# Kernel optimization log

Measured on AMD Instinct MI355X. Metric: run time of the kernel, lower is better.

## Reference

```python
import jax, jax.numpy as jnp
import numpy as np


def setup_inputs() -> dict:
    key = jax.random.key(0)
    k1, k2 = jax.random.split(key)
    b, c, h, w = 2, 128, 96, 128
    feature0 = jax.random.normal(k1, (b, c, h, w), dtype=jnp.float32)
    feature1 = jax.random.normal(k2, (b, c, h, w), dtype=jnp.float32)
    return {"feature0": feature0, "feature1": feature1, "local_radius": 4}


def reference(feature0, feature1, local_radius):
    # Faithful to the torch module: sample coords are base pixel coords + integer
    # window offsets, so align_corners=True bilinear grid_sample with zeros padding
    # reduces exactly to an integer gather with out-of-bounds masking.
    b, c, h, w = feature0.shape
    r = int(local_radius)
    # base pixel coords (x, y), matching coords_grid channel order
    ys, xs = jnp.meshgrid(jnp.arange(h, dtype=jnp.float32),
                          jnp.arange(w, dtype=jnp.float32), indexing='ij')  # [h,w]
    # window offsets; row-major over (dy, dx) like generate_window_grid reshape(-1,2)
    dy, dx = jnp.meshgrid(jnp.arange(-r, r + 1), jnp.arange(-r, r + 1), indexing='ij')
    dy = dy.reshape(-1).astype(jnp.float32)  # [K]
    dx = dx.reshape(-1).astype(jnp.float32)
    K = dx.shape[0]

    sample_x = xs[:, :, None] + dx  # [h,w,K]
    sample_y = ys[:, :, None] + dy
    valid = ((sample_x >= 0) & (sample_x <= w - 1) &
             (sample_y >= 0) & (sample_y <= h - 1))  # [h,w,K]

    cxi = jnp.clip(sample_x, 0, w - 1).astype(jnp.int32)
    cyi = jnp.clip(sample_y, 0, h - 1).astype(jnp.int32)
    # gather: [b,c,h,w,K]; zeros padding outside bounds
    window_feature = feature1[:, :, cyi, cxi] * valid.astype(feature1.dtype)

    # correlation: per-pixel [1,c] x [c,K]
    corr = jnp.einsum('bchw,bchwk->bhwk', feature0, window_feature) / (c ** 0.5)
    prob = jax.nn.softmax(corr, axis=-1)  # [b,h,w,K]

    # weighted coord sum -> correspondence, then flow = correspondence - coords
    corr_x = jnp.sum(prob * sample_x, axis=-1)  # [b,h,w]
    corr_y = jnp.sum(prob * sample_y, axis=-1)
    flow = jnp.stack([corr_x - xs, corr_y - ys], axis=1)  # [b,2,h,w]

    match_prob = prob.reshape(b, h * w, K)
    return flow, match_prob
```

## Files before the change

kernel.cpp:

```cpp
#include <hip/hip_runtime.h>
#include <math.h>

#define W_ 128
#define H_ 96
#define C_ 128
#define HW_ (H_ * W_)
#define K_ 81
#define FLOW_ELEMS (2 * 2 * H_ * W_)
#define TCOLS 32
#define TSTR 66

typedef __fp16 f16x8 __attribute__((ext_vector_type(8)));
typedef float  f32x4 __attribute__((ext_vector_type(4)));

__device__ __forceinline__ unsigned pack_pair(float a, float b) {
    return __builtin_bit_cast(unsigned, __builtin_amdgcn_cvt_pkrtz(a, b));
}

__global__ __launch_bounds__(192) void fused_kernel(const float* __restrict__ f0,
                                                    const float* __restrict__ f1,
                                                    float* __restrict__ out) {
    __shared__ unsigned tile[TCOLS * TSTR];
    __shared__ float corr_lds[3][16][85];
    __shared__ float pmax[4][49], psum[4][49], pfxb[4][49], pfyb[4][49];
    __shared__ float ibuf[48];

    const int t = threadIdx.x;
    const int ry = t >> 6, l = t & 63;
    const int L = (blockIdx.x & 7) * 64 + (blockIdx.x >> 3);
    const int b = L >> 8;
    const int rem = L & 255;
    const int ys = rem >> 3, xq = rem & 7;
    const int y0 = ys * 3;
    const int px0 = xq * 16;

    int g_off[2], lds_w[2];
    bool g_ok[2];
#pragma unroll
    for (int i = 0; i < 2; ++i) {
        const int s = i * 192 + t;
        const int cp = s / 6;
        const int q = s - cp * 6;
        const int x0 = px0 + 4 * q - 4;
        g_ok[i] = (x0 >= 0) && (x0 <= 124);
        g_off[i] = 2 * cp * HW_ + (g_ok[i] ? x0 : 0);
        lds_w[i] = (4 * q) * TSTR + cp;
    }
    const float* f1base = f1 + (size_t)b * C_ * HW_;

    const float scale = 0.08838834764831845f;
    f16x8 a[4];
    {
        const float* f0p = f0 + (size_t)b * C_ * HW_ + (size_t)(y0 + ry) * W_
                              + px0 + (l & 15);
#pragma unroll
        for (int kk = 0; kk < 4; ++kk) {
            f16x8 av;
#pragma unroll
            for (int j = 0; j < 8; ++j)
                av[j] = (__fp16)(f0p[(size_t)(kk * 32 + (l >> 4) * 8 + j) * HW_] * scale);
            a[kk] = av;
        }
    }

    auto LOADP = [&](int p, float4 (&va)[2], float4 (&vb)[2], bool& ok) {
        const int r = y0 - 4 + p;
        ok = (r >= 0) && (r < H_);
        const float* f1b = f1base + (size_t)(ok ? r : 0) * W_;
#pragma unroll
        for (int i = 0; i < 2; ++i) {
            float4 x = {0.f, 0.f, 0.f, 0.f}, y = {0.f, 0.f, 0.f, 0.f};
            if (ok && g_ok[i]) {
                x = *(const float4*)(f1b + g_off[i]);
                y = *(const float4*)(f1b + g_off[i] + HW_);
            }
            va[i] = x; vb[i] = y;
        }
    };
    auto WRITEP = [&](const float4 (&va)[2], const float4 (&vb)[2]) {
#pragma unroll
        for (int i = 0; i < 2; ++i) {
            tile[lds_w[i]]            = pack_pair(va[i].x, vb[i].x);
            tile[lds_w[i] + TSTR]     = pack_pair(va[i].y, vb[i].y);
            tile[lds_w[i] + 2 * TSTR] = pack_pair(va[i].z, vb[i].z);
            tile[lds_w[i] + 3 * TSTR] = pack_pair(va[i].w, vb[i].w);
        }
    };
    auto COMPUTE = [&](int dyi) {
        f32x4 accA = {0.f, 0.f, 0.f, 0.f}, accB = {0.f, 0.f, 0.f, 0.f};
#pragma unroll
        for (int kk = 0; kk < 4; ++kk) {
            const int off = kk * 16 + (l >> 4) * 4;
            {
                const int col = l & 15;
                const uint2 lo = *(const uint2*)&tile[col * TSTR + off];
                const uint2 hi = *(const uint2*)&tile[col * TSTR + off + 2];
                const uint4 u = {lo.x, lo.y, hi.x, hi.y};
                accA = __builtin_amdgcn_mfma_f32_16x16x32_f16(
                    a[kk], __builtin_bit_cast(f16x8, u), accA, 0, 0, 0);
            }
            {
                const int col = 16 + (l & 15);
                const uint2 lo = *(const uint2*)&tile[col * TSTR + off];
                const uint2 hi = *(const uint2*)&tile[col * TSTR + off + 2];
                const uint4 u = {lo.x, lo.y, hi.x, hi.y};
                accB = __builtin_amdgcn_mfma_f32_16x16x32_f16(
                    a[kk], __builtin_bit_cast(f16x8, u), accB, 0, 0, 0);
            }
        }
#pragma unroll
        for (int h = 0; h < 2; ++h) {
            const f32x4 acc = h ? accB : accA;
#pragma unroll
            for (int rg = 0; rg < 4; ++rg) {
                const int i2 = (l >> 4) * 4 + rg;
                const int j2 = h * 16 + (l & 15);
                const int dxw = j2 - i2;
                if (dxw >= 0 && dxw <= 8)
                    corr_lds[ry][i2][dyi * 9 + dxw] = acc[rg];
            }
        }
    };

    float4 vaA[2], vbA[2], vaB[2], vbB[2], vaC[2], vbC[2];
    bool okA, okB, okC;

    LOADP(0, vaA, vbA, okA);
    LOADP(1, vaB, vbB, okB);
    for (int i = t; i < 3 * 16 * 85; i += 192) (&corr_lds[0][0][0])[i] = 0.f;
    __syncthreads();

#define PHASE(p, VA, VB, OK, LP, NVA, NVB, NOK)                              \
    do {                                                                     \
        if (OK) WRITEP(VA, VB);                                              \
        __syncthreads();                                                     \
        if (LP <= 10) LOADP(LP, NVA, NVB, NOK);                              \
        const int dyi = (p) - ry;                                            \
        if (OK && dyi >= 0 && dyi <= 8) COMPUTE(dyi);                        \
        __syncthreads();                                                     \
    } while (0)

    PHASE(0, vaA, vbA, okA, 2, vaC, vbC, okC);
    PHASE(1, vaB, vbB, okB, 3, vaA, vbA, okA);
    PHASE(2, vaC, vbC, okC, 4, vaB, vbB, okB);
    PHASE(3, vaA, vbA, okA, 5, vaC, vbC, okC);
    PHASE(4, vaB, vbB, okB, 6, vaA, vbA, okA);
    PHASE(5, vaC, vbC, okC, 7, vaB, vbB, okB);
    PHASE(6, vaA, vbA, okA, 8, vaC, vbC, okC);
    PHASE(7, vaB, vbB, okB, 9, vaA, vbA, okA);
    PHASE(8, vaC, vbC, okC, 10, vaB, vbB, okB);
    PHASE(9, vaA, vbA, okA, 11, vaC, vbC, okC);
    PHASE(10, vaB, vbB, okB, 11, vaC, vbC, okC);
#undef PHASE

    {
        const int pxi = t % 48;
        const int part = t / 48;
        const int sry = pxi >> 4, spx = pxi & 15;
        float pm = -1e30f;
        for (int k = part; k < K_; k += 4)
            pm = fmaxf(pm, corr_lds[sry][spx][k]);
        pmax[part][pxi] = pm;
        __syncthreads();
        const float m = fmaxf(fmaxf(pmax[0][pxi], pmax[1][pxi]),
                              fmaxf(pmax[2][pxi], pmax[3][pxi]));
        float ps = 0.f, pfx = 0.f, pfy = 0.f;
        for (int k = part; k < K_; k += 4) {
            const float e = __expf(corr_lds[sry][spx][k] - m);
            corr_lds[sry][spx][k] = e;
            ps += e;
            pfx += e * (float)(k % 9 - 4);
            pfy += e * (float)(k / 9 - 4);
        }
        psum[part][pxi] = ps; pfxb[part][pxi] = pfx; pfyb[part][pxi] = pfy;
        __syncthreads();
        if (t < 48) {
            const float s = psum[0][t] + psum[1][t] + psum[2][t] + psum[3][t];
            const float inv = 1.f / s;
            ibuf[t] = inv;
            const float fx = pfxb[0][t] + pfxb[1][t] + pfxb[2][t] + pfxb[3][t];
            const float fy = pfyb[0][t] + pfyb[1][t] + pfyb[2][t] + pfyb[3][t];
            const int yy = y0 + (t >> 4);
            const int x = px0 + (t & 15);
            out[((size_t)(b * 2 + 0) * H_ + yy) * W_ + x] = fx * inv;
            out[((size_t)(b * 2 + 1) * H_ + yy) * W_ + x] = fy * inv;
        }
    }
    __syncthreads();

    float* outp = out + FLOW_ELEMS;
    for (int f = t; f < 48 * K_; f += 192) {
        const int pxi = f / K_;
        const int k = f - pxi * K_;
        const int yy = y0 + (pxi >> 4);
        const int x = px0 + (pxi & 15);
        outp[((size_t)b * HW_ + (size_t)yy * W_ + x) * K_ + k] =
            corr_lds[pxi >> 4][pxi & 15][k] * ibuf[pxi];
    }
}

extern "C" void kernel_launch(void* const* d_in, const int* in_sizes, int n_in,
                              void* d_out, int out_size, void* d_ws, size_t ws_size,
                              hipStream_t stream) {
    (void)in_sizes; (void)n_in; (void)out_size; (void)d_ws; (void)ws_size;
    const float* f0 = (const float*)d_in[0];
    const float* f1 = (const float*)d_in[1];
    float* out = (float*)d_out;

    fused_kernel<<<512, 192, 0, stream>>>(f0, f1, out);
}
```

Measured before the change: 22.65 us.

## Double-buffer LDS tile and deepen global prefetch to five rows

Makes the shared tile two buffers that alternate between phases, which removes the second barrier in each phase. It also raises the register prefetch depth from two rows to five, so global loads of f1 run further ahead of the MFMA compute. WRITEP now always writes, relying on LOADP zero-filling out-of-range rows, and compute is guarded by the row range instead. The cost is more registers (ten float4 pairs) and extra LDS, which may lower occupancy.

```diff
diff --git a/kernel.cpp b/kernel.cpp
--- a/kernel.cpp
+++ b/kernel.cpp
@@ -20,7 +20,7 @@
 __global__ __launch_bounds__(192) void fused_kernel(const float* __restrict__ f0,
                                                     const float* __restrict__ f1,
                                                     float* __restrict__ out) {
-    __shared__ unsigned tile[TCOLS * TSTR];
+    __shared__ unsigned tile[2][TCOLS * TSTR];
     __shared__ float corr_lds[3][16][85];
     __shared__ float pmax[4][49], psum[4][49], pfxb[4][49], pfyb[4][49];
     __shared__ float ibuf[48];
@@ -63,9 +63,9 @@
         }
     }
 
-    auto LOADP = [&](int p, float4 (&va)[2], float4 (&vb)[2], bool& ok) {
+    auto LOADP = [&](int p, float4 (&va)[2], float4 (&vb)[2]) {
         const int r = y0 - 4 + p;
-        ok = (r >= 0) && (r < H_);
+        const bool ok = (r >= 0) && (r < H_);
         const float* f1b = f1base + (size_t)(ok ? r : 0) * W_;
 #pragma unroll
         for (int i = 0; i < 2; ++i) {
@@ -77,32 +77,32 @@
             va[i] = x; vb[i] = y;
         }
     };
-    auto WRITEP = [&](const float4 (&va)[2], const float4 (&vb)[2]) {
+    auto WRITEP = [&](unsigned* tl, const float4 (&va)[2], const float4 (&vb)[2]) {
 #pragma unroll
         for (int i = 0; i < 2; ++i) {
-            tile[lds_w[i]]            = pack_pair(va[i].x, vb[i].x);
-            tile[lds_w[i] + TSTR]     = pack_pair(va[i].y, vb[i].y);
-            tile[lds_w[i] + 2 * TSTR] = pack_pair(va[i].z, vb[i].z);
-            tile[lds_w[i] + 3 * TSTR] = pack_pair(va[i].w, vb[i].w);
+            tl[lds_w[i]]            = pack_pair(va[i].x, vb[i].x);
+            tl[lds_w[i] + TSTR]     = pack_pair(va[i].y, vb[i].y);
+            tl[lds_w[i] + 2 * TSTR] = pack_pair(va[i].z, vb[i].z);
+            tl[lds_w[i] + 3 * TSTR] = pack_pair(va[i].w, vb[i].w);
         }
     };
-    auto COMPUTE = [&](int dyi) {
+    auto COMPUTE = [&](const unsigned* tl, int dyi) {
         f32x4 accA = {0.f, 0.f, 0.f, 0.f}, accB = {0.f, 0.f, 0.f, 0.f};
 #pragma unroll
         for (int kk = 0; kk < 4; ++kk) {
             const int off = kk * 16 + (l >> 4) * 4;
             {
                 const int col = l & 15;
-                const uint2 lo = *(const uint2*)&tile[col * TSTR + off];
-                const uint2 hi = *(const uint2*)&tile[col * TSTR + off + 2];
+                const uint2 lo = *(const uint2*)&tl[col * TSTR + off];
+                const uint2 hi = *(const uint2*)&tl[col * TSTR + off + 2];
                 const uint4 u = {lo.x, lo.y, hi.x, hi.y};
                 accA = __builtin_amdgcn_mfma_f32_16x16x32_f16(
                     a[kk], __builtin_bit_cast(f16x8, u), accA, 0, 0, 0);
             }
             {
                 const int col = 16 + (l & 15);
-                const uint2 lo = *(const uint2*)&tile[col * TSTR + off];
-                const uint2 hi = *(const uint2*)&tile[col * TSTR + off + 2];
+                const uint2 lo = *(const uint2*)&tl[col * TSTR + off];
+                const uint2 hi = *(const uint2*)&tl[col * TSTR + off + 2];
                 const uint4 u = {lo.x, lo.y, hi.x, hi.y};
                 accB = __builtin_amdgcn_mfma_f32_16x16x32_f16(
                     a[kk], __builtin_bit_cast(f16x8, u), accB, 0, 0, 0);
@@ -122,36 +122,41 @@
         }
     };
 
-    float4 vaA[2], vbA[2], vaB[2], vbB[2], vaC[2], vbC[2];
-    bool okA, okB, okC;
-
-    LOADP(0, vaA, vbA, okA);
-    LOADP(1, vaB, vbB, okB);
+    float4 va0[2], vb0[2], va1[2], vb1[2], va2[2], vb2[2],
+           va3[2], vb3[2], va4[2], vb4[2];
+
+    LOADP(0, va0, vb0);
+    LOADP(1, va1, vb1);
+    LOADP(2, va2, vb2);
+    LOADP(3, va3, vb3);
+    LOADP(4, va4, vb4);
     for (int i = t; i < 3 * 16 * 85; i += 192) (&corr_lds[0][0][0])[i] = 0.f;
     __syncthreads();
 
-#define PHASE(p, VA, VB, OK, LP, NVA, NVB, NOK)                              \
+#define PHASE(p, VA, VB)                                                     \
     do {                                                                     \
-        if (OK) WRITEP(VA, VB);                                              \
+        unsigned* tl = tile[(p) & 1];                                        \
+        WRITEP(tl, VA, VB);                                                  \
         __syncthreads();                                                     \
-        if (LP <= 10) LOADP(LP, NVA, NVB, NOK);                              \
+        if ((p) + 5 <= 10) LOADP((p) + 5, VA, VB);                           \
+        const int rr = y0 - 4 + (p);                                         \
         const int dyi = (p) - ry;                                            \
-        if (OK && dyi >= 0 && dyi <= 8) COMPUTE(dyi);                        \
-        __syncthreads();                                                     \
+        if (rr >= 0 && rr < H_ && dyi >= 0 && dyi <= 8) COMPUTE(tl, dyi);    \
     } while (0)
 
-    PHASE(0, vaA, vbA, okA, 2, vaC, vbC, okC);
-    PHASE(1, vaB, vbB, okB, 3, vaA, vbA, okA);
-    PHASE(2, vaC, vbC, okC, 4, vaB, vbB, okB);
-    PHASE(3, vaA, vbA, okA, 5, vaC, vbC, okC);
-    PHASE(4, vaB, vbB, okB, 6, vaA, vbA, okA);
-    PHASE(5, vaC, vbC, okC, 7, vaB, vbB, okB);
-    PHASE(6, vaA, vbA, okA, 8, vaC, vbC, okC);
-    PHASE(7, vaB, vbB, okB, 9, vaA, vbA, okA);
-    PHASE(8, vaC, vbC, okC, 10, vaB, vbB, okB);
-    PHASE(9, vaA, vbA, okA, 11, vaC, vbC, okC);
-    PHASE(10, vaB, vbB, okB, 11, vaC, vbC, okC);
+    PHASE(0, va0, vb0);
+    PHASE(1, va1, vb1);
+    PHASE(2, va2, vb2);
+    PHASE(3, va3, vb3);
+    PHASE(4, va4, vb4);
+    PHASE(5, va0, vb0);
+    PHASE(6, va1, vb1);
+    PHASE(7, va2, vb2);
+    PHASE(8, va3, vb3);
+    PHASE(9, va4, vb4);
+    PHASE(10, va0, vb0);
 #undef PHASE
+    __syncthreads();
 
     {
         const int pxi = t % 48;
```

After: 23.37 us. 1.03x slower.
